# Kernel tuning notes

Measured on AMD Instinct MI355X. Metric: run time of the kernel, lower is better.

## Reference

```python
import jax, jax.numpy as jnp
import numpy as np
from jax import lax

B, CIN, COUT, H, W, K = 8, 256, 256, 64, 64, 3
KK = K * K
PAD, STRIDE = 1, 1
EPS = 1e-5


def setup_inputs() -> dict:
    key = jax.random.key(0)
    k0, k1, k2 = jax.random.split(key, 3)
    x = jax.random.normal(k0, (B, CIN, H, W), jnp.float32)
    # offset/mask predicting conv: 3*K*K output channels (o1, o2, mask)
    w_off = jax.random.normal(k1, (3 * KK, CIN, K, K), jnp.float32) * 0.01
    b_off = jnp.zeros((3 * KK,), jnp.float32)
    # main deformable conv weight
    weight = jax.random.normal(k2, (COUT, CIN, K, K), jnp.float32) / np.sqrt(CIN * KK).astype(np.float32)
    bias = jnp.zeros((COUT,), jnp.float32)
    gamma = jnp.ones((COUT,), jnp.float32)
    beta = jnp.zeros((COUT,), jnp.float32)
    return {"x": x, "w_off": w_off, "b_off": b_off, "weight": weight,
            "bias": bias, "gamma": gamma, "beta": beta}


def _bilinear_sample(img, ph, pw):
    """img: [C,H,W]; ph,pw: [KK,H,W] float sample positions. Zero outside. -> [C,KK,H,W]"""
    h0 = jnp.floor(ph).astype(jnp.int32)
    w0 = jnp.floor(pw).astype(jnp.int32)
    h1, w1 = h0 + 1, w0 + 1
    lh = ph - h0.astype(ph.dtype)
    lw = pw - w0.astype(pw.dtype)
    hh, hw = 1.0 - lh, 1.0 - lw

    def corner(hi, wi):
        valid = (hi >= 0) & (hi < H) & (wi >= 0) & (wi < W)
        hc = jnp.clip(hi, 0, H - 1)
        wc = jnp.clip(wi, 0, W - 1)
        v = img[:, hc, wc]  # [C,KK,H,W]
        return v * valid.astype(img.dtype)[None]

    return (corner(h0, w0) * (hh * hw)[None] + corner(h0, w1) * (hh * lw)[None]
            + corner(h1, w0) * (lh * hw)[None] + corner(h1, w1) * (lh * lw)[None])


def _forward(x, w_off, b_off, weight, bias, gamma, beta):
    dn = ('NCHW', 'OIHW', 'NCHW')
    # offset/mask branch (standard conv)
    om = lax.conv_general_dilated(x, w_off, (STRIDE, STRIDE), ((PAD, PAD), (PAD, PAD)),
                                  dimension_numbers=dn) + b_off[None, :, None, None]
    o1, o2, m = jnp.split(om, 3, axis=1)
    offset = jnp.concatenate([o1, o2], axis=1)          # [B, 2*KK, H, W]
    off_h = offset[:, 0::2]                             # [B, KK, H, W] dy per tap
    off_w = offset[:, 1::2]                             # [B, KK, H, W] dx per tap
    mask = jax.nn.sigmoid(m)                            # [B, KK, H, W]

    taps = jnp.arange(KK)
    base_h = (taps // K - PAD).astype(jnp.float32)[:, None, None] \
        + (jnp.arange(H, dtype=jnp.float32) * STRIDE)[None, :, None]  # [KK,H,1]
    base_w = (taps % K - PAD).astype(jnp.float32)[:, None, None] \
        + (jnp.arange(W, dtype=jnp.float32) * STRIDE)[None, None, :]  # [KK,1,W]
    ph = base_h[None] + off_h                           # [B,KK,H,W]
    pw = base_w[None] + off_w

    sampled = jax.vmap(_bilinear_sample)(x, ph, pw)     # [B,CIN,KK,H,W]
    sampled = sampled * mask[:, None]                   # modulated (DCNv2)

    y = jnp.einsum('bckhw,ock->bohw', sampled, weight.reshape(COUT, CIN, KK))
    y = y + bias[None, :, None, None]

    # BatchNorm2d (training mode: batch statistics) + ReLU
    mean = y.mean(axis=(0, 2, 3))
    var = y.var(axis=(0, 2, 3))
    yn = (y - mean[None, :, None, None]) * lax.rsqrt(var + EPS)[None, :, None, None]
    out = jax.nn.relu(gamma[None, :, None, None] * yn + beta[None, :, None, None])
    return out


def reference(x, w_off, b_off, weight, bias, gamma, beta):
    return _forward(x, w_off, b_off, weight, bias, gamma, beta)
```

## Files before the change

### kernel.cpp

```cpp
#include <hip/hip_runtime.h>
#include <cstdint>

#define BB    8
#define CIN   256
#define COUT  256
#define HH    64
#define WW    64

typedef __attribute__((ext_vector_type(8))) short    s16x8;
typedef __attribute__((ext_vector_type(8))) unsigned short u16x8;
typedef __attribute__((ext_vector_type(4))) unsigned short u16x4;
typedef __attribute__((ext_vector_type(4))) float    f32x4;

__device__ __forceinline__ float bf2f(unsigned short u) {
    unsigned int v = ((unsigned int)u) << 16;
    return __builtin_bit_cast(float, v);
}
__device__ __forceinline__ unsigned short f2bf(float f) {
    unsigned int u = __builtin_bit_cast(unsigned int, f);
    unsigned int r = (u + 0x7FFFu + ((u >> 16) & 1u)) >> 16;
    return (unsigned short)r;
}
__device__ __forceinline__ unsigned short f2bf_rz(float f) {
    return (unsigned short)(__builtin_bit_cast(unsigned int, f) >> 16);
}

__global__ void k_pack(const float* __restrict__ x,
                       const float* __restrict__ w,
                       const float* __restrict__ woff,
                       unsigned short* __restrict__ xT,
                       unsigned short* __restrict__ wTk,
                       unsigned short* __restrict__ wofT,
                       float* __restrict__ gsum,
                       float* __restrict__ gssq) {
    int blk = blockIdx.x;
    int t = threadIdx.x;
    __shared__ float tile[64 * 65];
    if (blk == 0 && t < 256) { gsum[t] = 0.f; gssq[t] = 0.f; }
    if (blk < 2048) {
        int b    = blk & 7;
        int rest = blk >> 3;
        int h    = rest >> 2;
        int c0   = (rest & 3) * 64;
#pragma unroll
        for (int r = 0; r < 16; ++r) {
            int idx = t + r * 256;
            int i = idx >> 6, w_ = idx & 63;
            tile[i * 65 + w_] = x[(((b * 256 + c0 + i) * 64 + h) * 64) + w_];
        }
        __syncthreads();
#pragma unroll
        for (int r = 0; r < 2; ++r) {
            int idx = t + r * 256;
            int w_ = idx >> 3;
            int c8 = (idx & 7) * 8;
            u16x8 res;
#pragma unroll
            for (int k = 0; k < 8; ++k) res[k] = f2bf(tile[(c8 + k) * 65 + w_]);
            *reinterpret_cast<u16x8*>(&xT[((b * 64 + h) * 64 + w_) * 256 + c0 + c8]) = res;
        }
    } else if (blk < 4352) {
        int idx = (blk - 2048) * 256 + t;
        int j   = idx & 7;
        int q   = (idx >> 3) & 3;
        int o16 = (idx >> 5) & 15;
        int n16 = (idx >> 9) & 15;
        int kc  = (idx >> 13) & 7;
        int tp  = idx >> 16;
        int c = kc * 32 + q * 8 + j;
        int o = n16 * 16 + o16;
        wTk[idx] = f2bf(w[(o * 256 + c) * 9 + tp]);
    } else {
        int idx = (blk - 4352) * 256 + t;
        int c  = idx & 255;
        int j  = (idx >> 8) & 31;
        int tp = idx >> 13;
        wofT[idx] = f2bf((j < 27) ? woff[(j * 256 + c) * 9 + tp] : 0.f);
    }
}

__global__ __launch_bounds__(512, 4)
void k_main(const unsigned short* __restrict__ xT,
            const unsigned short* __restrict__ wTk,
            const unsigned short* __restrict__ wofT,
            const float* __restrict__ boffg,
            const float* __restrict__ bias,
            unsigned short* __restrict__ y16,
            float* __restrict__ gsum, float* __restrict__ gssq) {
    __shared__ __align__(16) char smem[76032];
    int blk = blockIdx.x;
    int b = blk & 7, h = blk >> 3;
    int pblk = b * 64 + h;
    int t = threadIdx.x;
    int lane = t & 63, wv = t >> 6;
    int lm = lane & 15, q = lane >> 4;
    const f32x4 FZ = {0.f, 0.f, 0.f, 0.f};

    {
        unsigned short* S3 = (unsigned short*)smem;
        float* PART = (float*)(smem + 53856);
        float* OMS  = (float*)(smem + 67584);
        f32x4 oacc0 = FZ, oacc1 = FZ;
        int myTile = wv & 3;
        int myKH   = wv >> 2;
        int p0w = myTile * 16;
        for (int cc = 0; cc < 2; ++cc) {
            __syncthreads();
            if (t < 96) {
                int rr = t >> 5, col = (t >> 4) & 1, c8 = (t & 15) * 8;
                u16x8 z = {0,0,0,0,0,0,0,0};
                *reinterpret_cast<u16x8*>(&S3[(rr * 66 + col * 65) * 136 + c8]) = z;
            }
#pragma unroll
            for (int r = 0; r < 6; ++r) {
                int v = t + r * 512;
                int rr = v >> 10, rem = v & 1023;
                int w_ = rem >> 4, c8 = (rem & 15) * 8;
                int hr = h + rr - 1;
                u16x8 d = {0,0,0,0,0,0,0,0};
                if (hr >= 0 && hr < 64)
                    d = *reinterpret_cast<const u16x8*>(xT + ((b * 64 + hr) * 64 + w_) * 256 + cc * 128 + c8);
                *reinterpret_cast<u16x8*>(&S3[(rr * 66 + w_ + 1) * 136 + c8]) = d;
            }
            __syncthreads();
            {
                int boff = cc * 128 + myKH * 64 + q * 8;
                s16x8 pb[4], nb[4];
                {
                    const unsigned short* wb = wofT + (0 * 32 + lm) * 256 + boff;
                    pb[0] = *reinterpret_cast<const s16x8*>(wb);
                    pb[1] = *reinterpret_cast<const s16x8*>(wb + 32);
                    pb[2] = *reinterpret_cast<const s16x8*>(wb + 16 * 256);
                    pb[3] = *reinterpret_cast<const s16x8*>(wb + 16 * 256 + 32);
                }
#pragma unroll
                for (int tp = 0; tp < 9; ++tp) {
                    if (tp < 8) {
                        const unsigned short* wb = wofT + ((tp + 1) * 32 + lm) * 256 + boff;
                        nb[0] = *reinterpret_cast<const s16x8*>(wb);
                        nb[1] = *reinterpret_cast<const s16x8*>(wb + 32);
                        nb[2] = *reinterpret_cast<const s16x8*>(wb + 16 * 256);
                        nb[3] = *reinterpret_cast<const s16x8*>(wb + 16 * 256 + 32);
                    }
                    int dh = tp / 3, dw_ = tp % 3;
                    int arow = (dh * 66 + p0w + lm + dw_) * 136 + myKH * 64 + q * 8;
                    s16x8 a0 = *reinterpret_cast<const s16x8*>(&S3[arow]);
                    s16x8 a1 = *reinterpret_cast<const s16x8*>(&S3[arow + 32]);
                    oacc0 = __builtin_amdgcn_mfma_f32_16x16x32_bf16(a0, pb[0], oacc0, 0, 0, 0);
                    oacc0 = __builtin_amdgcn_mfma_f32_16x16x32_bf16(a1, pb[1], oacc0, 0, 0, 0);
                    oacc1 = __builtin_amdgcn_mfma_f32_16x16x32_bf16(a0, pb[2], oacc1, 0, 0, 0);
                    oacc1 = __builtin_amdgcn_mfma_f32_16x16x32_bf16(a1, pb[3], oacc1, 0, 0, 0);
#pragma unroll
                    for (int i = 0; i < 4; ++i) pb[i] = nb[i];
                }
            }
        }
        __syncthreads();
        if (wv >= 4) {
#pragma unroll
            for (int i = 0; i < 4; ++i) {
                int prow = p0w + q * 4 + i;
                PART[prow * 33 + lm]      = oacc0[i];
                PART[prow * 33 + 16 + lm] = oacc1[i];
            }
        }
        __syncthreads();
        if (wv < 4) {
#pragma unroll
            for (int n = 0; n < 2; ++n) {
                int j = n * 16 + lm;
                float bj = (j < 27) ? boffg[j] : 0.f;
                f32x4 a = n ? oacc1 : oacc0;
#pragma unroll
                for (int i = 0; i < 4; ++i) {
                    int prow = p0w + q * 4 + i;
                    OMS[prow * 33 + j] = a[i] + PART[prow * 33 + j] + bj;
                }
            }
        }
        __syncthreads();
    }

    unsigned short* S = (unsigned short*)smem;
    float* OMS = (float*)(smem + 67584);
    f32x4 acc[4][4];
#pragma unroll
    for (int m = 0; m < 4; ++m)
#pragma unroll
        for (int n = 0; n < 4; ++n) acc[m][n] = FZ;

    if (wv >= 4) {
        int pw = wv - 4;
        int s  = lane & 7;
        int pA = pw * 16 + (lane >> 3);
        int pB = pA + 8;
        int rb = b * 4096;

        float wgA[4], wgB[4];
        int   adA[4], adB[4];

        auto setup = [&](int tp, int p, float* wgt, int* ad) {
            float oh = OMS[p * 33 + 2 * tp];
            float ow = OMS[p * 33 + 2 * tp + 1];
            float mv = OMS[p * 33 + 18 + tp];
            float mk = 1.f / (1.f + __expf(-mv));
            float ph = (float)(h + tp / 3 - 1) + oh;
            float pw_ = (float)(p + tp % 3 - 1) + ow;
            float fh0 = floorf(ph), fw0 = floorf(pw_);
            int ih0 = (int)fh0, iw0 = (int)fw0;
            float lh = ph - fh0, lw = pw_ - fw0;
            float hh = 1.f - lh, hw_ = 1.f - lw;
            bool vh0 = (ih0 >= 0) & (ih0 < 64);
            bool vh1 = (ih0 + 1 >= 0) & (ih0 + 1 < 64);
            bool vw0 = (iw0 >= 0) & (iw0 < 64);
            bool vw1 = (iw0 + 1 >= 0) & (iw0 + 1 < 64);
            wgt[0] = hh * hw_ * mk * (float)(vh0 & vw0);
            wgt[1] = hh * lw  * mk * (float)(vh0 & vw1);
            wgt[2] = lh * hw_ * mk * (float)(vh1 & vw0);
            wgt[3] = lh * lw  * mk * (float)(vh1 & vw1);
            int ch0 = min(max(ih0, 0), 63), ch1 = min(max(ih0 + 1, 0), 63);
            int cw0 = min(max(iw0, 0), 63), cw1 = min(max(iw0 + 1, 0), 63);
            ad[0] = ((rb + ch0 * 64 + cw0) * 256);
            ad[1] = ((rb + ch0 * 64 + cw1) * 256);
            ad[2] = ((rb + ch1 * 64 + cw0) * 256);
            ad[3] = ((rb + ch1 * 64 + cw1) * 256);
        };

        u16x8 rP[4], rQ[4];
        auto issueSet = [&](const int* ad, int j, u16x8* r) {
            int off = j * 64 + s * 8;
#pragma unroll
            for (int c = 0; c < 4; ++c)
                r[c] = *reinterpret_cast<const u16x8*>(xT + ad[c] + off);
        };
        auto blendSet = [&](int buf, int p, const float* wgt, int j, u16x8* r) {
            u16x8 res;
#pragma unroll
            for (int k = 0; k < 8; ++k) {
                float v = wgt[0] * bf2f(r[0][k]);
                v = fmaf(wgt[1], bf2f(r[1][k]), v);
                v = fmaf(wgt[2], bf2f(r[2][k]), v);
                v = fmaf(wgt[3], bf2f(r[3][k]), v);
                res[k] = f2bf_rz(v);
            }
            *reinterpret_cast<u16x8*>(&S[buf * 16896 + p * 264 + j * 64 + s * 8]) = res;
        };
        auto fillTap = [&](int tp, int buf) {
            setup(tp, pA, wgA, adA);
            setup(tp, pB, wgB, adB);
            issueSet(adA, 0, rP);
            issueSet(adA, 1, rQ);
            blendSet(buf, pA, wgA, 0, rP);  issueSet(adA, 2, rP);
            blendSet(buf, pA, wgA, 1, rQ);  issueSet(adA, 3, rQ);
            blendSet(buf, pA, wgA, 2, rP);  issueSet(adB, 0, rP);
            blendSet(buf, pA, wgA, 3, rQ);  issueSet(adB, 1, rQ);
            blendSet(buf, pB, wgB, 0, rP);  issueSet(adB, 2, rP);
            blendSet(buf, pB, wgB, 1, rQ);  issueSet(adB, 3, rQ);
            blendSet(buf, pB, wgB, 2, rP);
            blendSet(buf, pB, wgB, 3, rQ);
        };

        fillTap(0, 0);
        __syncthreads();
        for (int tp = 0; tp < 9; ++tp) {
            if (tp < 8) fillTap(tp + 1, (tp + 1) & 1);
            __syncthreads();
        }
    } else {
        __syncthreads();
        for (int tp = 0; tp < 9; ++tp) {
            const unsigned short* Sc = &S[(tp & 1) * 16896];
            const unsigned short* wtap = wTk + (size_t)tp * 65536
                                       + (size_t)(wv * 4) * 512 + lm * 32 + q * 8;
            s16x8 wbuf[2][4];
#pragma unroll
            for (int n = 0; n < 4; ++n)
                wbuf[0][n] = *reinterpret_cast<const s16x8*>(wtap + n * 512);
#pragma unroll
            for (int kc = 0; kc < 8; ++kc) {
                if (kc < 7) {
                    const unsigned short* wb = wtap + (kc + 1) * 8192;
#pragma unroll
                    for (int n = 0; n < 4; ++n)
                        wbuf[(kc + 1) & 1][n] = *reinterpret_cast<const s16x8*>(wb + n * 512);
                }
#pragma unroll
                for (int mt = 0; mt < 4; ++mt) {
                    s16x8 a = *reinterpret_cast<const s16x8*>(
                        &Sc[(mt * 16 + lm) * 264 + kc * 32 + q * 8]);
#pragma unroll
                    for (int n = 0; n < 4; ++n)
                        acc[mt][n] = __builtin_amdgcn_mfma_f32_16x16x32_bf16(
                            a, wbuf[kc & 1][n], acc[mt][n], 0, 0, 0);
                }
            }
            __syncthreads();
        }
    }

    if (wv < 4) {
        u16x4* yv = reinterpret_cast<u16x4*>(y16);
#pragma unroll
        for (int nt = 0; nt < 4; ++nt) {
            int o = wv * 64 + nt * 16 + lm;
            float bo = bias[o];
            float sacc = 0.f, ssacc = 0.f;
#pragma unroll
            for (int mt = 0; mt < 4; ++mt) {
                u16x4 st;
#pragma unroll
                for (int i = 0; i < 4; ++i) {
                    float v = acc[mt][nt][i] + bo;
                    st[i] = f2bf(v);
                    sacc += v; ssacc += v * v;
                }
                int idx4 = ((pblk * 4 + wv) * 16 + nt * 4 + mt) * 64 + lane;
                yv[idx4] = st;
            }
            sacc  += __shfl_xor(sacc, 16);
            sacc  += __shfl_xor(sacc, 32);
            ssacc += __shfl_xor(ssacc, 16);
            ssacc += __shfl_xor(ssacc, 32);
            if (q == 0) {
                atomicAdd(&gsum[o], sacc);
                atomicAdd(&gssq[o], ssacc);
            }
        }
    }
}

__global__ void k_bnrelu(const unsigned short* __restrict__ y16,
                         const float* __restrict__ gsum, const float* __restrict__ gssq,
                         const float* __restrict__ gamma, const float* __restrict__ beta,
                         float* __restrict__ out) {
    int blk = blockIdx.x;
    int b = blk & 7, h = blk >> 3;
    int pblk = b * 64 + h;
    __shared__ unsigned short T[64 * 257];
    __shared__ float sc[256], sh[256];
    int t = threadIdx.x;
    {
        const float n = 32768.f;
        float mean = gsum[t] / n;
        float var = gssq[t] / n - mean * mean;
        float inv = rsqrtf(var + 1e-5f);
        float s = gamma[t] * inv;
        sc[t] = s;
        sh[t] = beta[t] - mean * s;
    }
    const u16x4* yv = reinterpret_cast<const u16x4*>(y16) + pblk * 4096;
#pragma unroll
    for (int r = 0; r < 16; ++r) {
        int v = t + r * 256;
        u16x4 d = yv[v];
        int lane = v & 63, mt = (v >> 6) & 3, nt = (v >> 8) & 3, wvv = (v >> 10) & 3;
        int p = mt * 16 + (lane >> 4) * 4;
        int o = wvv * 64 + nt * 16 + (lane & 15);
        T[(p + 0) * 257 + o] = d[0];
        T[(p + 1) * 257 + o] = d[1];
        T[(p + 2) * 257 + o] = d[2];
        T[(p + 3) * 257 + o] = d[3];
    }
    __syncthreads();
    int w4   = (t & 15) * 4;
    int orow = t >> 4;
    float* obase = out + (size_t)b * (256 * 4096) + h * 64;
#pragma unroll
    for (int it = 0; it < 16; ++it) {
        int o = orow + it * 16;
        float scl = sc[o], shf = sh[o];
        float4 vo;
        vo.x = fmaxf(bf2f(T[(w4 + 0) * 257 + o]) * scl + shf, 0.f);
        vo.y = fmaxf(bf2f(T[(w4 + 1) * 257 + o]) * scl + shf, 0.f);
        vo.z = fmaxf(bf2f(T[(w4 + 2) * 257 + o]) * scl + shf, 0.f);
        vo.w = fmaxf(bf2f(T[(w4 + 3) * 257 + o]) * scl + shf, 0.f);
        *reinterpret_cast<float4*>(obase + (size_t)o * 4096 + w4) = vo;
    }
}

extern "C" void kernel_launch(void* const* d_in, const int* in_sizes, int n_in,
                              void* d_out, int out_size, void* d_ws, size_t ws_size,
                              hipStream_t stream) {
    const float* x      = (const float*)d_in[0];
    const float* w_off  = (const float*)d_in[1];
    const float* b_off  = (const float*)d_in[2];
    const float* weight = (const float*)d_in[3];
    const float* bias   = (const float*)d_in[4];
    const float* gamma  = (const float*)d_in[5];
    const float* beta   = (const float*)d_in[6];

    char* ws = (char*)d_ws;
    const size_t OFF_XT    = 0;
    const size_t OFF_WT    = OFF_XT + 16777216;
    const size_t OFF_WOFT  = OFF_WT + 1179648;
    const size_t OFF_Y16   = OFF_WOFT + 147456;
    const size_t OFF_SUM   = OFF_Y16 + 16777216;
    const size_t OFF_SUMSQ = OFF_SUM + 1024;

    unsigned short* xT   = (unsigned short*)(ws + OFF_XT);
    unsigned short* wTk  = (unsigned short*)(ws + OFF_WT);
    unsigned short* wofT = (unsigned short*)(ws + OFF_WOFT);
    unsigned short* y16  = (unsigned short*)(ws + OFF_Y16);
    float* gsum  = (float*)(ws + OFF_SUM);
    float* gssq  = (float*)(ws + OFF_SUMSQ);

    k_pack  <<<4640, 256, 0, stream>>>(x, weight, w_off, xT, wTk, wofT, gsum, gssq);
    k_main  <<< 512, 512, 0, stream>>>(xT, wTk, wofT, b_off, bias, y16, gsum, gssq);
    k_bnrelu<<< 512, 256, 0, stream>>>(y16, gsum, gssq, gamma, beta, (float*)d_out);
}
```

Measured before the change: 200.9 us.

## Transpose conv output in LDS inside main kernel, simplify BN-ReLU kernel

The main kernel now stages its bf16 output tile in shared memory and writes it to global in channel-major [o][w] order, so the intermediate is stored in the final layout. The BN+ReLU kernel no longer needs an LDS transpose. It splits each (b,h) row across four channel groups, giving 2048 blocks, and reads 16-byte vectors to write contiguous float4 pairs. The cost is an extra LDS pass and barrier at the end of the main kernel, and this relies on the reused smem buffer being large enough and free at that point.

```diff
diff --git a/kernel.cpp b/kernel.cpp
--- a/kernel.cpp
+++ b/kernel.cpp
@@ -298,8 +298,8 @@
         }
     }
 
+    unsigned short* T = (unsigned short*)smem;
     if (wv < 4) {
-        u16x4* yv = reinterpret_cast<u16x4*>(y16);
 #pragma unroll
         for (int nt = 0; nt < 4; ++nt) {
             int o = wv * 64 + nt * 16 + lm;
@@ -307,15 +307,12 @@
             float sacc = 0.f, ssacc = 0.f;
 #pragma unroll
             for (int mt = 0; mt < 4; ++mt) {
-                u16x4 st;
 #pragma unroll
                 for (int i = 0; i < 4; ++i) {
                     float v = acc[mt][nt][i] + bo;
-                    st[i] = f2bf(v);
+                    T[o * 68 + mt * 16 + q * 4 + i] = f2bf(v);
                     sacc += v; ssacc += v * v;
                 }
-                int idx4 = ((pblk * 4 + wv) * 16 + nt * 4 + mt) * 64 + lane;
-                yv[idx4] = st;
             }
             sacc  += __shfl_xor(sacc, 16);
             sacc  += __shfl_xor(sacc, 32);
@@ -327,54 +324,60 @@
             }
         }
     }
+    __syncthreads();
+    u16x4* yv = reinterpret_cast<u16x4*>(y16) + (size_t)pblk * 4096;
+#pragma unroll
+    for (int k = 0; k < 8; ++k) {
+        int u = t + k * 512;
+        int o = u >> 4, g2 = u & 15;
+        yv[o * 16 + g2] = *reinterpret_cast<const u16x4*>(&T[o * 68 + g2 * 4]);
+    }
 }
 
 __global__ void k_bnrelu(const unsigned short* __restrict__ y16,
                          const float* __restrict__ gsum, const float* __restrict__ gssq,
                          const float* __restrict__ gamma, const float* __restrict__ beta,
                          float* __restrict__ out) {
-    int blk = blockIdx.x;
-    int b = blk & 7, h = blk >> 3;
+    int i = blockIdx.x;
+    int t = threadIdx.x;
+    int b    = i & 7;
+    int rest = i >> 3;
+    int h    = rest & 63;
+    int o0   = (rest >> 6) * 64;
     int pblk = b * 64 + h;
-    __shared__ unsigned short T[64 * 257];
-    __shared__ float sc[256], sh[256];
-    int t = threadIdx.x;
-    {
-        const float n = 32768.f;
-        float mean = gsum[t] / n;
-        float var = gssq[t] / n - mean * mean;
+    __shared__ float sc[64], sh[64];
+    if (t < 64) {
+        int o = o0 + t;
+        const float invn = 1.f / 32768.f;
+        float mean = gsum[o] * invn;
+        float var = gssq[o] * invn - mean * mean;
         float inv = rsqrtf(var + 1e-5f);
-        float s = gamma[t] * inv;
+        float s = gamma[o] * inv;
         sc[t] = s;
-        sh[t] = beta[t] - mean * s;
-    }
-    const u16x4* yv = reinterpret_cast<const u16x4*>(y16) + pblk * 4096;
-#pragma unroll
-    for (int r = 0; r < 16; ++r) {
-        int v = t + r * 256;
-        u16x4 d = yv[v];
-        int lane = v & 63, mt = (v >> 6) & 3, nt = (v >> 8) & 3, wvv = (v >> 10) & 3;
-        int p = mt * 16 + (lane >> 4) * 4;
-        int o = wvv * 64 + nt * 16 + (lane & 15);
-        T[(p + 0) * 257 + o] = d[0];
-        T[(p + 1) * 257 + o] = d[1];
-        T[(p + 2) * 257 + o] = d[2];
-        T[(p + 3) * 257 + o] = d[3];
+        sh[t] = beta[o] - mean * s;
     }
     __syncthreads();
-    int w4   = (t & 15) * 4;
-    int orow = t >> 4;
-    float* obase = out + (size_t)b * (256 * 4096) + h * 64;
-#pragma unroll
-    for (int it = 0; it < 16; ++it) {
-        int o = orow + it * 16;
-        float scl = sc[o], shf = sh[o];
-        float4 vo;
-        vo.x = fmaxf(bf2f(T[(w4 + 0) * 257 + o]) * scl + shf, 0.f);
-        vo.y = fmaxf(bf2f(T[(w4 + 1) * 257 + o]) * scl + shf, 0.f);
-        vo.z = fmaxf(bf2f(T[(w4 + 2) * 257 + o]) * scl + shf, 0.f);
-        vo.w = fmaxf(bf2f(T[(w4 + 3) * 257 + o]) * scl + shf, 0.f);
-        *reinterpret_cast<float4*>(obase + (size_t)o * 4096 + w4) = vo;
+    const u16x8* yv = reinterpret_cast<const u16x8*>(
+        y16 + ((size_t)pblk * 256 + o0) * 64);
+    float* obase = out + ((size_t)b * 256 + o0) * 4096 + h * 64;
+#pragma unroll
+    for (int r = 0; r < 2; ++r) {
+        int c = t + r * 256;
+        int row = c >> 3, g = c & 7;
+        u16x8 d = yv[row * 8 + g];
+        float scl = sc[row], shf = sh[row];
+        float4 v0, v1;
+        v0.x = fmaxf(bf2f(d[0]) * scl + shf, 0.f);
+        v0.y = fmaxf(bf2f(d[1]) * scl + shf, 0.f);
+        v0.z = fmaxf(bf2f(d[2]) * scl + shf, 0.f);
+        v0.w = fmaxf(bf2f(d[3]) * scl + shf, 0.f);
+        v1.x = fmaxf(bf2f(d[4]) * scl + shf, 0.f);
+        v1.y = fmaxf(bf2f(d[5]) * scl + shf, 0.f);
+        v1.z = fmaxf(bf2f(d[6]) * scl + shf, 0.f);
+        v1.w = fmaxf(bf2f(d[7]) * scl + shf, 0.f);
+        float* op = obase + row * 4096 + g * 8;
+        *reinterpret_cast<float4*>(op)     = v0;
+        *reinterpret_cast<float4*>(op + 4) = v1;
     }
 }
 
@@ -406,5 +409,5 @@
 
     k_pack  <<<4640, 256, 0, stream>>>(x, weight, w_off, xT, wTk, wofT, gsum, gssq);
     k_main  <<< 512, 512, 0, stream>>>(xT, wTk, wofT, b_off, bias, y16, gsum, gssq);
-    k_bnrelu<<< 512, 256, 0, stream>>>(y16, gsum, gssq, gamma, beta, (float*)d_out);
-}
+    k_bnrelu<<<2048, 256, 0, stream>>>(y16, gsum, gssq, gamma, beta, (float*)d_out);
+}
```

New measurement: 202.2 us. Within noise of the previous version (+0.7%).
